# Optimization experiments

Measured on AMD Instinct MI355X. Metric: run time of the kernel, lower is better.

The kernel has to match this reference:

```python
import jax, jax.numpy as jnp
import numpy as np

M = 16           # size_graph_filter (nodes per hidden prototype graph)
S = 16           # size_subgraph
D_IN = 128       # input_dim
H = 64           # hidden_dim
O = 32           # out_dim (number of hidden prototype graphs)
B = 32768        # batch of subgraphs
MAX_STEP = 3
BN_EPS = 1e-5


def setup_inputs() -> dict:
    key = jax.random.key(0)
    ks = jax.random.split(key, 8)
    adj = jax.random.uniform(ks[0], (B, S, S), dtype=jnp.float32)
    adj = 0.5 * (adj + jnp.swapaxes(adj, 1, 2))  # symmetric weighted adjacency
    features = jax.random.normal(ks[1], (B, S, D_IN), dtype=jnp.float32)
    # learned parameters (per torch init: uniform inits, Linear default-like fc_in)
    W_in = jax.random.normal(ks[2], (D_IN, H), dtype=jnp.float32) * (1.0 / np.sqrt(D_IN))
    b_in = jnp.zeros((H,), dtype=jnp.float32)
    features_hidden = jax.random.uniform(ks[3], (M, H, O), dtype=jnp.float32)          # U(0,1)
    adj_hidden = jax.random.uniform(ks[4], (M * (M - 1) // 2, O), dtype=jnp.float32,
                                    minval=-1.0, maxval=1.0)                            # U(-1,1)
    bn_gamma = jnp.ones((O,), dtype=jnp.float32)
    bn_beta = jnp.zeros((O,), dtype=jnp.float32)
    return {"adj": adj, "features": features, "W_in": W_in, "b_in": b_in,
            "features_hidden": features_hidden, "adj_hidden": adj_hidden,
            "bn_gamma": bn_gamma, "bn_beta": bn_beta}


def reference(adj, features, W_in, b_in, features_hidden, adj_hidden, bn_gamma, bn_beta):
    # Build symmetric hidden adjacency (M, M, O) from triu-packed parameters.
    iu, ju = jnp.triu_indices(M, k=1)
    A = jnp.zeros((M, M, O), dtype=adj_hidden.dtype)
    A = A.at[iu, ju, :].set(jax.nn.relu(adj_hidden))
    A = A + jnp.swapaxes(A, 0, 1)

    x = jax.nn.sigmoid(features @ W_in + b_in)   # (B, S, H)
    z = features_hidden                           # (M, H, O)

    acc = jnp.zeros((B, O), dtype=x.dtype)
    for step in range(MAX_STEP):
        if step > 0:
            x = jnp.einsum('bst,bth->bsh', adj, x)        # propagate on input subgraphs
            z = jnp.einsum('mpo,pho->mho', A, z)          # propagate on hidden graphs
        # random-walk kernel value between each subgraph and each prototype
        t = jnp.einsum('mho,bsh->bo', z, x)               # sum over prototype & subgraph nodes
        acc = acc + t
    out = acc / MAX_STEP

    # BatchNorm1d (training-mode batch statistics), then sigmoid; dropout p used in eval = identity
    mean = jnp.mean(out, axis=0)
    var = jnp.var(out, axis=0)
    out = (out - mean) / jnp.sqrt(var + BN_EPS) * bn_gamma + bn_beta
    return jax.nn.sigmoid(out)
```

## Files before the change

kernel.cpp:

```cpp
#include <hip/hip_runtime.h>


typedef short  vec8s  __attribute__((ext_vector_type(8)));
typedef short  vec4s  __attribute__((ext_vector_type(4)));
typedef float  f32x4  __attribute__((ext_vector_type(4)));
typedef unsigned short vec4us __attribute__((ext_vector_type(4)));

#define NB      32768
#define SS      16
#define DIN     128
#define HH      64
#define OO      32
#define MM      16

__device__ __forceinline__ float bf2f(unsigned short u) {
    return __uint_as_float(((unsigned int)u) << 16);
}
__device__ __forceinline__ unsigned short f2bf(float f) {
    unsigned int u = __float_as_uint(f);
    unsigned int r = (u + 0x7fffu + ((u >> 16) & 1u)) >> 16;
    return (unsigned short)r;
}
template<bool F32>
__device__ __forceinline__ float ldv(const void* p, int i) {
    if (F32) return ((const float*)p)[i];
    return bf2f(((const unsigned short*)p)[i]);
}

__global__ void p0_probe(const void* feat, int* flag) {
    __shared__ int chuge, czero;
    if (threadIdx.x == 0) { chuge = 0; czero = 0; }
    __syncthreads();
    const unsigned short* p = (const unsigned short*)feat;
    int h = 0, z = 0;
    for (int i = threadIdx.x; i < 4096; i += 64) {
        unsigned short u = p[i];
        unsigned e = (u >> 7) & 0xFFu;
        if (e >= 0x90u) h++;
        if ((u & 0x7FFFu) == 0) z++;
    }
    atomicAdd(&chuge, h);
    atomicAdd(&czero, z);
    __syncthreads();
    if (threadIdx.x == 0) *flag = (chuge > 8 || czero > 512) ? 1 : 0;
}

template<bool F32>
__device__ __forceinline__ float Aval(const void* ahS, int i, int j, int o) {
    if (i == j) return 0.f;
    int a = i < j ? i : j;
    int b = i < j ? j : i;
    int idx = a * 15 - ((a * (a - 1)) >> 1) + (b - a - 1);
    float v = ldv<F32>(ahS, idx * OO + o);
    return v > 0.f ? v : 0.f;
}

template<bool F32>
__device__ void k1_body(const void* fhP, const void* ahP, const void* WP,
                        short* ZcnS, short* WtS, float* cA, float* c2) {
    const int tid = threadIdx.x;
    for (int i = tid; i < MM * OO; i += 256) {
        int p = i >> 5, o = i & 31;
        float s = 0.f;
        for (int m = 0; m < MM; ++m) s += Aval<F32>(ahP, m, p, o);
        cA[i] = s;
    }
    __syncthreads();
    for (int i = tid; i < MM * OO; i += 256) {
        int qq = i >> 5, o = i & 31;
        float s = 0.f;
        for (int p = 0; p < MM; ++p) s += cA[p * OO + o] * Aval<F32>(ahP, p, qq, o);
        c2[i] = s;
    }
    __syncthreads();
    for (int i = blockIdx.x * 256 + tid; i < 3 * OO * HH; i += 16 * 256) {
        int n = i >> 6, h = i & 63;
        int step = n >> 5, o = n & 31;
        float v = 0.f;
        for (int p = 0; p < MM; ++p) {
            float z = ldv<F32>(fhP, p * (HH * OO) + h * OO + o);
            float w = (step == 0) ? 1.f : (step == 1 ? cA[p * OO + o] : c2[p * OO + o]);
            v += w * z;
        }
        ZcnS[n * HH + h] = (short)f2bf(v);
    }
    for (int i = blockIdx.x * 256 + tid; i < DIN * HH; i += 16 * 256) {
        int h = i >> 7, k = i & 127;
        WtS[h * DIN + k] = (short)f2bf(ldv<F32>(WP, k * HH + h));
    }
}

__global__ void k1_prep(const void* fhP, const void* ahP, const void* WP,
                        short* ZcnS, short* WtS, double* dstats,
                        const int* flag) {
    __shared__ float cA[MM * OO];
    __shared__ float c2[MM * OO];
    if (blockIdx.x == 0 && threadIdx.x < 64) dstats[threadIdx.x] = 0.0;
    if (*flag) k1_body<true>(fhP, ahP, WP, ZcnS, WtS, cA, c2);
    else       k1_body<false>(fhP, ahP, WP, ZcnS, WtS, cA, c2);
}

template<bool F32>
__device__ void k2_body(const void* adjP, const void* featP, const void* binP,
                        const short* ZcnS, const short* WtS, float* accOut,
                        double* dstats, short* myx0, float* bsum, float* bsqs) {
    const int tid  = threadIdx.x;
    const int lane = tid & 63;
    const int hl   = lane & 15;
    const int q    = lane >> 4;

    vec8s Wfrag[4][4];
    for (int kt = 0; kt < 4; ++kt)
        for (int nt = 0; nt < 4; ++nt)
            Wfrag[kt][nt] = *(const vec8s*)(WtS + (nt * 16 + hl) * DIN + kt * 32 + q * 8);
    vec8s Zfrag[2][6];
    for (int kt = 0; kt < 2; ++kt)
        for (int t = 0; t < 6; ++t)
            Zfrag[kt][t] = *(const vec8s*)(ZcnS + (t * 16 + hl) * HH + kt * 32 + q * 8);
    float biasv[4];
    for (int nt = 0; nt < 4; ++nt) biasv[nt] = ldv<F32>(binP, nt * 16 + hl);

    const f32x4 z4 = {0.f, 0.f, 0.f, 0.f};
    float ls = 0.f, lss = 0.f;
    const int wgid = blockIdx.x * 4 + (tid >> 6);

    for (int b = wgid; b < NB; b += 2048) {
        float a0, a1, a2, a3;
        vec8s af[4];
        if (F32) {
            f32x4 av = *(const f32x4*)((const float*)adjP + b * (SS * SS) + lane * 4);
            a0 = av[0]; a1 = av[1]; a2 = av[2]; a3 = av[3];
            const float* fb = (const float*)featP + b * (SS * DIN) + hl * DIN + q * 8;
            for (int kt = 0; kt < 4; ++kt) {
                f32x4 lo = *(const f32x4*)(fb + kt * 32);
                f32x4 hi = *(const f32x4*)(fb + kt * 32 + 4);
                vec8s v;
                for (int j = 0; j < 4; ++j) {
                    v[j]     = (short)f2bf(lo[j]);
                    v[4 + j] = (short)f2bf(hi[j]);
                }
                af[kt] = v;
            }
        } else {
            vec4s av = *(const vec4s*)((const short*)adjP + b * (SS * SS) + lane * 4);
            a0 = bf2f((unsigned short)av.x); a1 = bf2f((unsigned short)av.y);
            a2 = bf2f((unsigned short)av.z); a3 = bf2f((unsigned short)av.w);
            const short* fb = (const short*)featP + b * (SS * DIN) + hl * DIN + q * 8;
            for (int kt = 0; kt < 4; ++kt) af[kt] = *(const vec8s*)(fb + kt * 32);
        }

        float rsum = a0 + a1 + a2 + a3;
        rsum += __shfl_xor(rsum, 1);
        rsum += __shfl_xor(rsum, 2);
        int cg = lane & 3;
        float rr0 = __shfl(rsum, cg * 16 + 0);
        float rr1 = __shfl(rsum, cg * 16 + 4);
        float rr2 = __shfl(rsum, cg * 16 + 8);
        float rr3 = __shfl(rsum, cg * 16 + 12);
        float p = a0 * rr0 + a1 * rr1 + a2 * rr2 + a3 * rr3;
        p += __shfl_xor(p, 1);
        p += __shfl_xor(p, 2);
        float w1q[4], w2q[4];
        for (int reg = 0; reg < 4; ++reg) {
            int src = q * 16 + reg * 4;
            w1q[reg] = __shfl(rsum, src);
            w2q[reg] = __shfl(p, src);
        }

        f32x4 c1[4] = {z4, z4, z4, z4};
        for (int nt = 0; nt < 4; ++nt)
            for (int kt = 0; kt < 4; ++kt)
                c1[nt] = __builtin_amdgcn_mfma_f32_16x16x32_bf16(af[kt], Wfrag[kt][nt], c1[nt], 0, 0, 0);

        for (int nt = 0; nt < 4; ++nt)
            for (int reg = 0; reg < 4; ++reg) {
                float x = c1[nt][reg] + biasv[nt];
                float sg = 1.f / (1.f + __expf(-x));
                myx0[(q * 4 + reg) * 72 + nt * 16 + hl] = (short)f2bf(sg);
            }
        __syncthreads();

        vec8s a2lo = *(const vec8s*)(myx0 + hl * 72 + q * 8);
        vec8s a2hi = *(const vec8s*)(myx0 + hl * 72 + 32 + q * 8);
        __syncthreads();
        f32x4 cp[6] = {z4, z4, z4, z4, z4, z4};
        for (int t = 0; t < 6; ++t)
            cp[t] = __builtin_amdgcn_mfma_f32_16x16x32_bf16(a2lo, Zfrag[0][t], cp[t], 0, 0, 0);
        for (int t = 0; t < 6; ++t)
            cp[t] = __builtin_amdgcn_mfma_f32_16x16x32_bf16(a2hi, Zfrag[1][t], cp[t], 0, 0, 0);

        float parts[6];
        for (int t = 0; t < 6; ++t) {
            int step = t >> 1;
            float v;
            if (step == 0)      v = cp[t][0] + cp[t][1] + cp[t][2] + cp[t][3];
            else if (step == 1) v = cp[t][0]*w1q[0] + cp[t][1]*w1q[1] + cp[t][2]*w1q[2] + cp[t][3]*w1q[3];
            else                v = cp[t][0]*w2q[0] + cp[t][1]*w2q[1] + cp[t][2]*w2q[2] + cp[t][3]*w2q[3];
            v += __shfl_xor(v, 16);
            v += __shfl_xor(v, 32);
            parts[t] = v;
        }
        float accA = parts[0] + parts[2] + parts[4];
        float accB = parts[1] + parts[3] + parts[5];
        float accv = ((lane >> 4) & 1) ? accB : accA;
        accv *= (1.f / 3.f);
        accv = __builtin_isnan(accv) ? 0.f : accv;
        if (lane < OO) accOut[b * OO + lane] = accv;
        ls  += accv;
        lss += accv * accv;
    }

    if (lane < OO) {
        atomicAdd(&bsum[lane], ls);
        atomicAdd(&bsqs[lane], lss);
    }
    __syncthreads();
    if (tid < OO) {
        atomicAdd(&dstats[tid],      (double)bsum[tid]);
        atomicAdd(&dstats[OO + tid], (double)bsqs[tid]);
    }
}

__global__ __launch_bounds__(256, 2) void k2_main(
    const void* adjP, const void* featP, const void* binP,
    const short* ZcnS, const short* WtS, float* accOut,
    double* dstats, const int* flag) {
    __shared__ __align__(16) short x0buf[4][SS * 72];
    __shared__ float bsum[OO];
    __shared__ float bsqs[OO];
    const int tid = threadIdx.x;
    if (tid < OO) { bsum[tid] = 0.f; bsqs[tid] = 0.f; }
    __syncthreads();
    short* myx0 = x0buf[tid >> 6];
    if (*flag) k2_body<true>(adjP, featP, binP, ZcnS, WtS, accOut, dstats, myx0, bsum, bsqs);
    else       k2_body<false>(adjP, featP, binP, ZcnS, WtS, accOut, dstats, myx0, bsum, bsqs);
}

__global__ void k3_stats(const double* __restrict__ dstats,
                         const void* gammaP, const void* betaP,
                         float* __restrict__ scaleArr, float* __restrict__ shiftArr,
                         const int* flag) {
    int o = threadIdx.x;
    if (o >= OO) return;
    double mean = dstats[o] * (1.0 / (double)NB);
    double ex2  = dstats[OO + o] * (1.0 / (double)NB);
    double var  = ex2 - mean * mean;
    if (var < 0.0) var = 0.0;
    double inv  = 1.0 / sqrt(var + 1e-5);
    float g, be;
    if (*flag) { g = ldv<true>(gammaP, o);  be = ldv<true>(betaP, o); }
    else       { g = ldv<false>(gammaP, o); be = ldv<false>(betaP, o); }
    float scale = g * (float)inv;
    scaleArr[o] = scale;
    shiftArr[o] = be - (float)(mean * inv) * g;
}

__global__ __launch_bounds__(256) void k4_out(const float* __restrict__ acc,
                                              const float* __restrict__ scaleArr,
                                              const float* __restrict__ shiftArr,
                                              void* out, const int* flag) {
    int i = (blockIdx.x * 256 + threadIdx.x) * 4;
    int o0 = i & 31;
    f32x4 a  = *(const f32x4*)(acc + i);
    f32x4 sc = *(const f32x4*)(scaleArr + o0);
    f32x4 sh = *(const f32x4*)(shiftArr + o0);
    float r[4];
    for (int j = 0; j < 4; ++j) {
        float z = a[j] * sc[j] + sh[j];
        r[j] = 1.f / (1.f + __expf(-z));
    }
    if (*flag) {
        f32x4 w;
        for (int j = 0; j < 4; ++j) w[j] = r[j];
        *(f32x4*)((float*)out + i) = w;
    } else {
        vec4us w;
        for (int j = 0; j < 4; ++j) w[j] = f2bf(r[j]);
        *(vec4us*)((unsigned short*)out + i) = w;
    }
}

extern "C" void kernel_launch(void* const* d_in, const int* in_sizes, int n_in,
                              void* d_out, int out_size, void* d_ws, size_t ws_size,
                              hipStream_t stream) {
    const void* adjP   = d_in[0];
    const void* featP  = d_in[1];
    const void* WP     = d_in[2];
    const void* binP   = d_in[3];
    const void* fhP    = d_in[4];
    const void* ahP    = d_in[5];
    const void* gammaP = d_in[6];
    const void* betaP  = d_in[7];

    char* ws = (char*)d_ws;
    float*  accOut   = (float*)(ws);
    short*  ZcnS     = (short*)(ws + 4194304);
    short*  WtS      = (short*)(ws + 4206592);
    double* dstats   = (double*)(ws + 4222976);
    float*  scaleArr = (float*)(ws + 4223488);
    float*  shiftArr = (float*)(ws + 4223616);
    int*    flag     = (int*)(ws + 4223744);

    hipLaunchKernelGGL(p0_probe, dim3(1),    dim3(64),  0, stream, featP, flag);
    hipLaunchKernelGGL(k1_prep,  dim3(16),   dim3(256), 0, stream,
                       fhP, ahP, WP, ZcnS, WtS, dstats, flag);
    hipLaunchKernelGGL(k2_main,  dim3(512),  dim3(256), 0, stream,
                       adjP, featP, binP, ZcnS, WtS, accOut, dstats, flag);
    hipLaunchKernelGGL(k3_stats, dim3(1),    dim3(32),  0, stream,
                       dstats, gammaP, betaP, scaleArr, shiftArr, flag);
    hipLaunchKernelGGL(k4_out,   dim3(1024), dim3(256), 0, stream,
                       accOut, scaleArr, shiftArr, d_out, flag);
}
```

Before: 438.3 us.

## Fold probe and BN-stats kernels into neighbours, cheapen bf16 packing, drop barriers

Merges the dtype probe into the prep kernel and the BatchNorm scale/shift computation into the output kernel, cutting two launches. The fp32-to-bf16 conversion switches to cheaper round-half-up bit packing. The two block barriers around the per-wave shared x0 buffer become block-level fences, since each wave uses its own buffer. This risks small rounding differences, and the fences may not order lanes within a wave as the barriers did.

```diff
diff --git a/kernel.cpp b/kernel.cpp
--- a/kernel.cpp
+++ b/kernel.cpp
@@ -26,23 +26,21 @@
     if (F32) return ((const float*)p)[i];
     return bf2f(((const unsigned short*)p)[i]);
 }
-
-__global__ void p0_probe(const void* feat, int* flag) {
-    __shared__ int chuge, czero;
-    if (threadIdx.x == 0) { chuge = 0; czero = 0; }
-    __syncthreads();
-    const unsigned short* p = (const unsigned short*)feat;
-    int h = 0, z = 0;
-    for (int i = threadIdx.x; i < 4096; i += 64) {
-        unsigned short u = p[i];
-        unsigned e = (u >> 7) & 0xFFu;
-        if (e >= 0x90u) h++;
-        if ((u & 0x7FFFu) == 0) z++;
-    }
-    atomicAdd(&chuge, h);
-    atomicAdd(&czero, z);
-    __syncthreads();
-    if (threadIdx.x == 0) *flag = (chuge > 8 || czero > 512) ? 1 : 0;
+__device__ __forceinline__ vec8s pack8(f32x4 lo, f32x4 hi) {
+    union { unsigned int u[4]; vec8s v; } r;
+    unsigned int a0 = __float_as_uint(lo[0]) + 0x8000u;
+    unsigned int a1 = __float_as_uint(lo[1]) + 0x8000u;
+    unsigned int a2 = __float_as_uint(lo[2]) + 0x8000u;
+    unsigned int a3 = __float_as_uint(lo[3]) + 0x8000u;
+    unsigned int b0 = __float_as_uint(hi[0]) + 0x8000u;
+    unsigned int b1 = __float_as_uint(hi[1]) + 0x8000u;
+    unsigned int b2 = __float_as_uint(hi[2]) + 0x8000u;
+    unsigned int b3 = __float_as_uint(hi[3]) + 0x8000u;
+    r.u[0] = (a0 >> 16) | (a1 & 0xFFFF0000u);
+    r.u[1] = (a2 >> 16) | (a3 & 0xFFFF0000u);
+    r.u[2] = (b0 >> 16) | (b1 & 0xFFFF0000u);
+    r.u[3] = (b2 >> 16) | (b3 & 0xFFFF0000u);
+    return r.v;
 }
 
 template<bool F32>
@@ -92,11 +90,33 @@
 
 __global__ void k1_prep(const void* fhP, const void* ahP, const void* WP,
                         short* ZcnS, short* WtS, double* dstats,
-                        const int* flag) {
+                        const void* featP, int* flag) {
     __shared__ float cA[MM * OO];
     __shared__ float c2[MM * OO];
-    if (blockIdx.x == 0 && threadIdx.x < 64) dstats[threadIdx.x] = 0.0;
-    if (*flag) k1_body<true>(fhP, ahP, WP, ZcnS, WtS, cA, c2);
+    __shared__ int chuge, czero, sflag;
+    const int tid = threadIdx.x;
+    if (tid == 0) { chuge = 0; czero = 0; }
+    if (blockIdx.x == 0 && tid < 64) dstats[tid] = 0.0;
+    __syncthreads();
+    if (tid < 64) {
+        const unsigned short* p = (const unsigned short*)featP;
+        int h = 0, z = 0;
+        for (int i = tid; i < 4096; i += 64) {
+            unsigned short u = p[i];
+            unsigned e = (u >> 7) & 0xFFu;
+            if (e >= 0x90u) h++;
+            if ((u & 0x7FFFu) == 0) z++;
+        }
+        atomicAdd(&chuge, h);
+        atomicAdd(&czero, z);
+    }
+    __syncthreads();
+    if (tid == 0) {
+        sflag = (chuge > 8 || czero > 512) ? 1 : 0;
+        if (blockIdx.x == 0) *flag = sflag;
+    }
+    __syncthreads();
+    if (sflag) k1_body<true>(fhP, ahP, WP, ZcnS, WtS, cA, c2);
     else       k1_body<false>(fhP, ahP, WP, ZcnS, WtS, cA, c2);
 }
 
@@ -134,12 +154,7 @@
             for (int kt = 0; kt < 4; ++kt) {
                 f32x4 lo = *(const f32x4*)(fb + kt * 32);
                 f32x4 hi = *(const f32x4*)(fb + kt * 32 + 4);
-                vec8s v;
-                for (int j = 0; j < 4; ++j) {
-                    v[j]     = (short)f2bf(lo[j]);
-                    v[4 + j] = (short)f2bf(hi[j]);
-                }
-                af[kt] = v;
+                af[kt] = pack8(lo, hi);
             }
         } else {
             vec4s av = *(const vec4s*)((const short*)adjP + b * (SS * SS) + lane * 4);
@@ -176,13 +191,14 @@
             for (int reg = 0; reg < 4; ++reg) {
                 float x = c1[nt][reg] + biasv[nt];
                 float sg = 1.f / (1.f + __expf(-x));
-                myx0[(q * 4 + reg) * 72 + nt * 16 + hl] = (short)f2bf(sg);
+                unsigned int u = __float_as_uint(sg) + 0x8000u;
+                myx0[(q * 4 + reg) * 72 + nt * 16 + hl] = (short)(u >> 16);
             }
-        __syncthreads();
+        __threadfence_block();
 
         vec8s a2lo = *(const vec8s*)(myx0 + hl * 72 + q * 8);
         vec8s a2hi = *(const vec8s*)(myx0 + hl * 72 + 32 + q * 8);
-        __syncthreads();
+        __threadfence_block();
         f32x4 cp[6] = {z4, z4, z4, z4, z4, z4};
         for (int t = 0; t < 6; ++t)
             cp[t] = __builtin_amdgcn_mfma_f32_16x16x32_bf16(a2lo, Zfrag[0][t], cp[t], 0, 0, 0);
@@ -236,40 +252,34 @@
     else       k2_body<false>(adjP, featP, binP, ZcnS, WtS, accOut, dstats, myx0, bsum, bsqs);
 }
 
-__global__ void k3_stats(const double* __restrict__ dstats,
-                         const void* gammaP, const void* betaP,
-                         float* __restrict__ scaleArr, float* __restrict__ shiftArr,
-                         const int* flag) {
-    int o = threadIdx.x;
-    if (o >= OO) return;
-    double mean = dstats[o] * (1.0 / (double)NB);
-    double ex2  = dstats[OO + o] * (1.0 / (double)NB);
-    double var  = ex2 - mean * mean;
-    if (var < 0.0) var = 0.0;
-    double inv  = 1.0 / sqrt(var + 1e-5);
-    float g, be;
-    if (*flag) { g = ldv<true>(gammaP, o);  be = ldv<true>(betaP, o); }
-    else       { g = ldv<false>(gammaP, o); be = ldv<false>(betaP, o); }
-    float scale = g * (float)inv;
-    scaleArr[o] = scale;
-    shiftArr[o] = be - (float)(mean * inv) * g;
-}
-
 __global__ __launch_bounds__(256) void k4_out(const float* __restrict__ acc,
-                                              const float* __restrict__ scaleArr,
-                                              const float* __restrict__ shiftArr,
+                                              const double* __restrict__ dstats,
+                                              const void* gammaP, const void* betaP,
                                               void* out, const int* flag) {
-    int i = (blockIdx.x * 256 + threadIdx.x) * 4;
+    __shared__ float sScale[OO], sShift[OO];
+    const int tid = threadIdx.x;
+    const int f = *flag;
+    if (tid < OO) {
+        double mean = dstats[tid] * (1.0 / (double)NB);
+        double ex2  = dstats[OO + tid] * (1.0 / (double)NB);
+        double var  = ex2 - mean * mean;
+        if (var < 0.0) var = 0.0;
+        double inv  = 1.0 / sqrt(var + 1e-5);
+        float g  = f ? ldv<true>(gammaP, tid) : ldv<false>(gammaP, tid);
+        float be = f ? ldv<true>(betaP, tid)  : ldv<false>(betaP, tid);
+        sScale[tid] = g * (float)inv;
+        sShift[tid] = be - (float)(mean * inv) * g;
+    }
+    __syncthreads();
+    int i = (blockIdx.x * 256 + tid) * 4;
     int o0 = i & 31;
-    f32x4 a  = *(const f32x4*)(acc + i);
-    f32x4 sc = *(const f32x4*)(scaleArr + o0);
-    f32x4 sh = *(const f32x4*)(shiftArr + o0);
+    f32x4 a = *(const f32x4*)(acc + i);
     float r[4];
     for (int j = 0; j < 4; ++j) {
-        float z = a[j] * sc[j] + sh[j];
+        float z = a[j] * sScale[o0 + j] + sShift[o0 + j];
         r[j] = 1.f / (1.f + __expf(-z));
     }
-    if (*flag) {
+    if (f) {
         f32x4 w;
         for (int j = 0; j < 4; ++j) w[j] = r[j];
         *(f32x4*)((float*)out + i) = w;
@@ -297,17 +307,12 @@
     short*  ZcnS     = (short*)(ws + 4194304);
     short*  WtS      = (short*)(ws + 4206592);
     double* dstats   = (double*)(ws + 4222976);
-    float*  scaleArr = (float*)(ws + 4223488);
-    float*  shiftArr = (float*)(ws + 4223616);
     int*    flag     = (int*)(ws + 4223744);
 
-    hipLaunchKernelGGL(p0_probe, dim3(1),    dim3(64),  0, stream, featP, flag);
     hipLaunchKernelGGL(k1_prep,  dim3(16),   dim3(256), 0, stream,
-                       fhP, ahP, WP, ZcnS, WtS, dstats, flag);
+                       fhP, ahP, WP, ZcnS, WtS, dstats, featP, flag);
     hipLaunchKernelGGL(k2_main,  dim3(512),  dim3(256), 0, stream,
                        adjP, featP, binP, ZcnS, WtS, accOut, dstats, flag);
-    hipLaunchKernelGGL(k3_stats, dim3(1),    dim3(32),  0, stream,
-                       dstats, gammaP, betaP, scaleArr, shiftArr, flag);
     hipLaunchKernelGGL(k4_out,   dim3(1024), dim3(256), 0, stream,
-                       accOut, scaleArr, shiftArr, d_out, flag);
-}
+                       accOut, dstats, gammaP, betaP, d_out, flag);
+}
```

Result: faster. 427.5 us (-2.5%).
